# Optimization experiments

Measured on AMD Instinct MI355X. Metric: run time of the kernel, lower is better.

Reference implementation:

```python
import jax, jax.numpy as jnp
import numpy as np

OFFSETS = (1, 2, 4, 8, 16, 64, 96, 192, 384, 512, 768, 1024)
J = 12
J_LARGE = 8  # offsets with index >= 4 use phase rotation


def _shift(x, d):
    """Return x shifted so out[..., n, :] = x[..., n-d, :]; zeros where n < d.
    Shift is along axis 2 (the sequence axis of [B,H,N,...])."""
    pad = [(0, 0)] * x.ndim
    pad[2] = (d, 0)
    return jnp.pad(x, pad)[:, :, : x.shape[2]]


def setup_inputs() -> dict:
    key = jax.random.key(0)
    ks = jax.random.split(key, 9)
    B, H, N, HD = 2, 16, 4096, 64
    f = jnp.float32
    q = jax.random.normal(ks[0], (B, H, N, HD), f)
    k = jax.random.normal(ks[1], (B, H, N, HD), f)
    v = jax.random.normal(ks[2], (B, H, N, HD), f)
    pb = jax.random.normal(ks[3], (J, H), f) * 0.1          # per-offset per-head score bias
    se = jax.random.normal(ks[4], (J, HD), f) * 0.1         # per-offset score embedding
    phase_base = jax.random.normal(ks[5], (J_LARGE, H, 2), f) * 0.1
    phase_gain = jax.random.normal(ks[6], (J_LARGE, H, 2), f) * 0.1
    y_pre = jax.random.normal(ks[7], (B, H, N, 2), f)       # query-side phase features
    z_pre = jax.random.normal(ks[8], (B, H, N, 2), f)       # key-side phase features
    return dict(q=q, k=k, v=v, pb=pb, se=se, phase_base=phase_base,
                phase_gain=phase_gain, y_pre=y_pre, z_pre=z_pre)


def reference(q, k, v, pb, se, phase_base, phase_gain, y_pre, z_pre):
    B, H, N, HD = q.shape
    sc = 1.0 / float(np.sqrt(HD))
    n_idx = jnp.arange(N)

    # --- scores over the J fixed causal offsets: s_i[n] = (q_n . (k_{n-d} + se_i)) * sc + pb[i,h]
    scores = []
    for i, d in enumerate(OFFSETS):
        ks_ = _shift(k, d)  # key at n - d
        s = (jnp.einsum('bhnd,bhnd->bhn', q, ks_)
             + jnp.einsum('bhnd,d->bhn', q, se[i])) * sc
        s = s + pb[i][None, :, None]
        valid = (n_idx >= d)[None, None, :]
        scores.append(jnp.where(valid, s, -jnp.inf))
    scores = jnp.stack(scores, axis=-1)  # [B,H,N,J]

    lse = jax.nn.logsumexp(scores, axis=-1)            # [B,H,N]
    safe_lse = jnp.where(jnp.isfinite(lse), lse, 0.0)  # rows with no valid offset -> alpha = 0
    alpha = jnp.exp(scores - safe_lse[..., None])      # [B,H,N,J]; -inf scores give exactly 0

    # --- weighted sum of (phase-rotated) values
    out = jnp.zeros_like(q)
    for i, d in enumerate(OFFSETS):
        vs = _shift(v, d)  # value at n - d: [B,H,N,HD]
        if i >= 4:
            pi = i - 4
            zs = _shift(z_pre, d)  # key-side phase features at n - d: [B,H,N,2]
            # theta_p = base[pi,h,p] + gain[pi,h,p] * y_pre[n,p] * z_pre[n-d,p]
            theta = (phase_base[pi][None, :, None, :]
                     + phase_gain[pi][None, :, None, :] * y_pre * zs)  # [B,H,N,2]
            c, s_ = jnp.cos(theta), jnp.sin(theta)
            v0, v1, v2, v3 = vs[..., 0], vs[..., 1], vs[..., 2], vs[..., 3]
            rot = jnp.stack([c[..., 0] * v0 - s_[..., 0] * v1,
                             s_[..., 0] * v0 + c[..., 0] * v1,
                             c[..., 1] * v2 - s_[..., 1] * v3,
                             s_[..., 1] * v2 + c[..., 1] * v3], axis=-1)
            vs = jnp.concatenate([rot, vs[..., 4:]], axis=-1)
        out = out + alpha[..., i:i + 1] * vs
    return out
```

## Files before the change

### kernel.cpp

```cpp
#include <hip/hip_runtime.h>


namespace {

constexpr int J   = 12;
constexpr int B_  = 2;
constexpr int H_  = 16;
constexpr int N_  = 4096;
constexpr int HD_ = 64;
constexpr int OFFS[J] = {1, 2, 4, 8, 16, 64, 96, 192, 384, 512, 768, 1024};
constexpr int T_  = 64;
constexpr int W_  = 80;

using f32x4 = __attribute__((ext_vector_type(4))) float;
using f32x2 = __attribute__((ext_vector_type(2))) float;

#define GLOAD4(dst, off, base)                                              \
    asm volatile("global_load_dwordx4 %0, %1, %2"                           \
                 : "=v"(dst) : "v"(off), "s"(base) : "memory")
#define GLOAD2(dst, off, base)                                              \
    asm volatile("global_load_dwordx2 %0, %1, %2"                           \
                 : "=v"(dst) : "v"(off), "s"(base) : "memory")

#define VMWAIT(N)                                                           \
    asm volatile("s_waitcnt vmcnt(" #N ")" ::: "memory");                   \
    __builtin_amdgcn_sched_barrier(0)

template <int CTRL>
__device__ __forceinline__ float dpp_add(float x) {
    int s = __builtin_amdgcn_update_dpp(0, __builtin_bit_cast(int, x),
                                        CTRL, 0xF, 0xF, false);
    return x + __builtin_bit_cast(float, s);
}

#define ISSUEA(nn, QR, KR, YP, ZL) do {                                     \
    const int nA_ = (nn);                                                   \
    const uint32_t rbA_ = ((uint32_t)nA_ << 8) + gbl;                       \
    GLOAD4(QR, rbA_, qb);                                                   \
    _Pragma("unroll")                                                       \
    for (int i = 5; i < J; ++i) {                                           \
        const uint32_t oA_ = (nA_ >= OFFS[i])                               \
            ? (rbA_ - ((uint32_t)OFFS[i] << 8)) : gbl;                      \
        GLOAD4(KR[i - 5], oA_, kb);                                         \
    }                                                                       \
    const uint32_t nb8A_ = (uint32_t)nA_ << 3;                              \
    GLOAD2(YP, nb8A_, yb);                                                  \
    const uint32_t zoA_ = (nA_ >= dl) ? ((uint32_t)(nA_ - dl) << 3) : 0u;   \
    GLOAD2(ZL, zoA_, zb);                                                   \
} while (0)

#define ITERBODY(NVAL, TOPN, TAILN, PREF, QR, KR, YP, ZL, QRN, KRN, YPN, ZLN) \
do {                                                                        \
    const int n_ = (NVAL);                                                  \
    const uint32_t rowb_ = ((uint32_t)n_ << 8) + gbl;                       \
    VMWAIT(TOPN);                                   \
    const int rbase_ = n_ - P + 16;                        \
    float p_[J];                                                            \
    _Pragma("unroll")                                                       \
    for (int i = 0; i < 5; ++i) {                                           \
        const f32x4 kk  = kS[(rbase_ - OFFS[i]) * 16 + grp];                \
        const f32x4 seg = seS[i * 16 + grp];                                \
        float t = QR.x * (kk.x + seg.x);                                    \
        t = fmaf(QR.y, kk.y + seg.y, t);                                    \
        t = fmaf(QR.z, kk.z + seg.z, t);                                    \
        p_[i] = fmaf(QR.w, kk.w + seg.w, t);                                \
    }                                                                       \
    _Pragma("unroll")                                                       \
    for (int i = 5; i < J; ++i) {                                           \
        const f32x4 kk  = KR[i - 5];                                        \
        const f32x4 seg = seS[i * 16 + grp];                                \
        float t = QR.x * (kk.x + seg.x);                                    \
        t = fmaf(QR.y, kk.y + seg.y, t);                                    \
        t = fmaf(QR.z, kk.z + seg.z, t);                                    \
        p_[i] = fmaf(QR.w, kk.w + seg.w, t);                                \
    }                                                                       \
                  \
    f32x4 vr_[7];                                                           \
    _Pragma("unroll")                                                       \
    for (int i = 5; i < J; ++i) {                                           \
        const uint32_t oB_ = (n_ >= OFFS[i])                                \
            ? (rowb_ - ((uint32_t)OFFS[i] << 8)) : gbl;                     \
        GLOAD4(vr_[i - 5], oB_, vb);                                        \
    }                                                                       \
    f32x4 vx_;                                                              \
    const uint32_t vxo_ = (n_ >= dl) ? ((uint32_t)(n_ - dl) << 8) : 0u;     \
    GLOAD4(vx_, vxo_, vb);                                                  \
    if (PREF) { ISSUEA(n_ + 4, QRN, KRN, YPN, ZLN); }                       \
          \
    _Pragma("unroll")                                                       \
    for (int i = 0; i < J; ++i) {                                           \
        p_[i] = dpp_add<0xB1>(p_[i]);      \
        p_[i] = dpp_add<0x4E>(p_[i]);      \
        p_[i] = dpp_add<0x124>(p_[i]);                       \
        p_[i] = dpp_add<0x128>(p_[i]);                       \
    }                                                                       \
    float e_[J];                                                            \
    float sum_ = 0.f;                                                       \
    _Pragma("unroll")                                                       \
    for (int i = 0; i < J; ++i) {                                           \
        const float si = fmaf(p_[i], 0.125f, pbh[i]);                       \
        e_[i] = (n_ >= OFFS[i]) ? __expf(si) : 0.f;                         \
        sum_ += e_[i];                                                      \
    }                                                                       \
    VMWAIT(TAILN);                  \
                \
    const float s01_ = (t8 & 1) ? e_[5]  : e_[4];                           \
    const float s23_ = (t8 & 1) ? e_[7]  : e_[6];                           \
    const float s45_ = (t8 & 1) ? e_[9]  : e_[8];                           \
    const float s67_ = (t8 & 1) ? e_[11] : e_[10];                          \
    const float sA_  = (t8 & 2) ? s23_ : s01_;                              \
    const float sB_  = (t8 & 2) ? s67_ : s45_;                              \
    const float esel_ = (t8 & 4) ? sB_ : sA_;                               \
    const float th0_ = fmaf(pgn.x, YP.x * ZL.x, pbs.x);                     \
    const float th1_ = fmaf(pgn.y, YP.y * ZL.y, pbs.y);                     \
    const float c0_ = __cosf(th0_), s0_ = __sinf(th0_);                     \
    const float c1_ = __cosf(th1_), s1_ = __sinf(th1_);                     \
    f32x4 cx_;                                                              \
    cx_.x = esel_ * (c0_ * vx_.x - s0_ * vx_.y);                            \
    cx_.y = esel_ * (s0_ * vx_.x + c0_ * vx_.y);                            \
    cx_.z = esel_ * (c1_ * vx_.z - s1_ * vx_.w);                            \
    cx_.w = esel_ * (s1_ * vx_.z + c1_ * vx_.w);                            \
    cx_.x = dpp_add<0xB1>(cx_.x);  cx_.y = dpp_add<0xB1>(cx_.y);            \
    cx_.z = dpp_add<0xB1>(cx_.z);  cx_.w = dpp_add<0xB1>(cx_.w);            \
    cx_.x = dpp_add<0x4E>(cx_.x);  cx_.y = dpp_add<0x4E>(cx_.y);            \
    cx_.z = dpp_add<0x4E>(cx_.z);  cx_.w = dpp_add<0x4E>(cx_.w);            \
    cx_.x = dpp_add<0x124>(cx_.x); cx_.y = dpp_add<0x124>(cx_.y);           \
    cx_.z = dpp_add<0x124>(cx_.z); cx_.w = dpp_add<0x124>(cx_.w);           \
                     \
    float4 accl_ = make_float4(0.f, 0.f, 0.f, 0.f);                         \
    _Pragma("unroll")                                                       \
    for (int i = 0; i < 4; ++i) {                                           \
        const f32x4 vv = vS[(rbase_ - OFFS[i]) * 16 + grp];                 \
        accl_.x = fmaf(e_[i], vv.x, accl_.x);                               \
        accl_.y = fmaf(e_[i], vv.y, accl_.y);                               \
        accl_.z = fmaf(e_[i], vv.z, accl_.z);                               \
        accl_.w = fmaf(e_[i], vv.w, accl_.w);                               \
    }                                                                       \
    float4 acch_ = accl_;                                                   \
    {                                                                       \
        const f32x4 vv = vS[(rbase_ - 16) * 16 + grp];                      \
        acch_.x = fmaf(e_[4], vv.x, acch_.x);                               \
        acch_.y = fmaf(e_[4], vv.y, acch_.y);                               \
        acch_.z = fmaf(e_[4], vv.z, acch_.z);                               \
        acch_.w = fmaf(e_[4], vv.w, acch_.w);                               \
    }                                                                       \
    _Pragma("unroll")                                                       \
    for (int i = 5; i < J; ++i) {                                           \
        acch_.x = fmaf(e_[i], vr_[i - 5].x, acch_.x);                       \
        acch_.y = fmaf(e_[i], vr_[i - 5].y, acch_.y);                       \
        acch_.z = fmaf(e_[i], vr_[i - 5].z, acch_.z);                       \
        acch_.w = fmaf(e_[i], vr_[i - 5].w, acch_.w);                       \
    }                                                                       \
    const bool lo_ = (grp == 0);                                            \
    float4 acc_;                                                            \
    acc_.x = lo_ ? accl_.x + cx_.x : acch_.x;                               \
    acc_.y = lo_ ? accl_.y + cx_.y : acch_.y;                               \
    acc_.z = lo_ ? accl_.z + cx_.z : acch_.z;                               \
    acc_.w = lo_ ? accl_.w + cx_.w : acch_.w;                               \
    float4 res_;                                                            \
    if (n_ >= 1) {                                                          \
        const float inv_ = __builtin_amdgcn_rcpf(sum_);                     \
        res_ = make_float4(acc_.x * inv_, acc_.y * inv_,                    \
                           acc_.z * inv_, acc_.w * inv_);                   \
    } else {                                                                \
        res_ = make_float4(0.f, 0.f, 0.f, 0.f);                             \
    }                                                                       \
    *(float4*)(ob + rowb_) = res_;        \
} while (0)

__global__ __launch_bounds__(256, 3) void dsqg_kernel(
    const float* __restrict__ q, const float* __restrict__ k,
    const float* __restrict__ v, const float* __restrict__ pb,
    const float* __restrict__ se, const float* __restrict__ phase_base,
    const float* __restrict__ phase_gain, const float* __restrict__ y_pre,
    const float* __restrict__ z_pre, float* __restrict__ out)
{
    __shared__ f32x4 kS[W_ * 16];
    __shared__ f32x4 vS[W_ * 16];
    __shared__ f32x4 seS[J * 16];

    const int raw = blockIdx.x;
    const int per = gridDim.x >> 3;
    const int wid = (raw & 7) * per + (raw >> 3);

    const int bh  = wid >> 6;
    const int blk = wid & 63;
    const int h   = bh & (H_ - 1);
    const int P   = blk * T_;

    const int tid  = threadIdx.x;
    const int lane = tid & 63;
    const int wave = tid >> 6;
    const int grp  = lane & 15;
    const int sub  = lane >> 4;

    if (tid < J * 16) seS[tid] = ((const f32x4*)se)[tid];

    const size_t bhbytes = (size_t)bh * (N_ * HD_ * 4);
    const char* qb = (const char*)q + bhbytes;
    const char* kb = (const char*)k + bhbytes;
    const char* vb = (const char*)v + bhbytes;
    char*       ob = (char*)out + bhbytes;
    const char* yb = (const char*)y_pre + (size_t)bh * (N_ * 8);
    const char* zb = (const char*)z_pre + (size_t)bh * (N_ * 8);

    {
        const int r0 = P - 16;
#pragma unroll
        for (int t = 0; t < (W_ * 16) / 256; ++t) {
            const int idx = t * 256 + tid;
            const int row = idx >> 4;
            const int col = idx & 15;
            int gr = r0 + row;
            gr = gr < 0 ? 0 : gr;
            const uint32_t go = ((uint32_t)gr << 8) + ((uint32_t)col << 4);
            kS[idx] = *(const f32x4*)(kb + go);
            vS[idx] = *(const f32x4*)(vb + go);
        }
    }

    const int t8  = grp & 7;
    const int d01 = (t8 & 1) ? 64   : 16;
    const int d23 = (t8 & 1) ? 192  : 96;
    const int d45 = (t8 & 1) ? 512  : 384;
    const int d67 = (t8 & 1) ? 1024 : 768;
    const int dA  = (t8 & 2) ? d23 : d01;
    const int dB  = (t8 & 2) ? d67 : d45;
    const int dl  = (t8 & 4) ? dB : dA;

    const uint32_t pofs = (uint32_t)(t8 * H_ + h) << 3;
    const f32x2 pbs = *(const f32x2*)((const char*)phase_base + pofs);
    const f32x2 pgn = *(const f32x2*)((const char*)phase_gain + pofs);
    float pbh[J];
#pragma unroll
    for (int i = 0; i < J; ++i) pbh[i] = pb[i * H_ + h];

    asm volatile("" :: "v"(pbs.x), "v"(pbs.y), "v"(pgn.x), "v"(pgn.y));
    asm volatile("" :: "v"(pbh[0]), "v"(pbh[1]), "v"(pbh[2]), "v"(pbh[3]),
                       "v"(pbh[4]), "v"(pbh[5]), "v"(pbh[6]), "v"(pbh[7]),
                       "v"(pbh[8]), "v"(pbh[9]), "v"(pbh[10]), "v"(pbh[11]));

    __syncthreads();

    const uint32_t gbl = (uint32_t)grp << 4;
    const int n0 = P + wave * 16 + sub;

    f32x4 qrA, qrB;
    f32x4 krA[7], krB[7];
    f32x2 ypA, ypB, zlA, zlB;

    ISSUEA(n0, qrA, krA, ypA, zlA);

    ITERBODY(n0,      2, 10, 1, qrA, krA, ypA, zlA, qrB, krB, ypB, zlB);
    ITERBODY(n0 + 4,  3, 10, 1, qrB, krB, ypB, zlB, qrA, krA, ypA, zlA);
    ITERBODY(n0 + 8,  3, 10, 1, qrA, krA, ypA, zlA, qrB, krB, ypB, zlB);
    ITERBODY(n0 + 12, 3,  0, 0, qrB, krB, ypB, zlB, qrA, krA, ypA, zlA);
}

}

extern "C" void kernel_launch(void* const* d_in, const int* in_sizes, int n_in,
                              void* d_out, int out_size, void* d_ws, size_t ws_size,
                              hipStream_t stream) {
    const float* q          = (const float*)d_in[0];
    const float* k          = (const float*)d_in[1];
    const float* v          = (const float*)d_in[2];
    const float* pb         = (const float*)d_in[3];
    const float* se         = (const float*)d_in[4];
    const float* phase_base = (const float*)d_in[5];
    const float* phase_gain = (const float*)d_in[6];
    const float* y_pre      = (const float*)d_in[7];
    const float* z_pre      = (const float*)d_in[8];
    float* out              = (float*)d_out;

    const int positions = B_ * H_ * N_;
    const int blocks    = positions / T_;
    dsqg_kernel<<<blocks, 256, 0, stream>>>(q, k, v, pb, se, phase_base,
                                            phase_gain, y_pre, z_pre, out);
}
```

Measured before the change: 173.7 us.

## Enlarge tiles and LDS halo so offsets up to 96 read K/V from shared memory

Raises the per-block tile from 64 to 128 positions, runs 512 threads per block, and widens the staged K/V halo to 96 rows. Offsets 64 and 96 now read keys and values from LDS instead of global memory, and some lanes fetch the rotated value from LDS. The row interleaving across waves and the prefetch stride change to match. The aim is fewer global K/V loads per position and better reuse. The cost is a larger dynamic LDS footprint (about 114 KB per block), which lowers occupancy, plus a bigger halo load per block.

```diff
diff --git a/kernel.cpp b/kernel.cpp
--- a/kernel.cpp
+++ b/kernel.cpp
@@ -9,8 +9,11 @@
 constexpr int N_  = 4096;
 constexpr int HD_ = 64;
 constexpr int OFFS[J] = {1, 2, 4, 8, 16, 64, 96, 192, 384, 512, 768, 1024};
-constexpr int T_  = 64;
-constexpr int W_  = 80;
+constexpr int T_   = 128;
+constexpr int HALO = 96;
+constexpr int W_   = T_ + HALO;
+constexpr int LDS_KV = W_ * 16 * 16;
+constexpr int LDS_TOTAL = 2 * LDS_KV + J * 16 * 16;
 
 using f32x4 = __attribute__((ext_vector_type(4))) float;
 using f32x2 = __attribute__((ext_vector_type(2))) float;
@@ -38,10 +41,10 @@
     const uint32_t rbA_ = ((uint32_t)nA_ << 8) + gbl;                       \
     GLOAD4(QR, rbA_, qb);                                                   \
     _Pragma("unroll")                                                       \
-    for (int i = 5; i < J; ++i) {                                           \
+    for (int i = 7; i < J; ++i) {                                           \
         const uint32_t oA_ = (nA_ >= OFFS[i])                               \
             ? (rbA_ - ((uint32_t)OFFS[i] << 8)) : gbl;                      \
-        GLOAD4(KR[i - 5], oA_, kb);                                         \
+        GLOAD4(KR[i - 7], oA_, kb);                                         \
     }                                                                       \
     const uint32_t nb8A_ = (uint32_t)nA_ << 3;                              \
     GLOAD2(YP, nb8A_, yb);                                                  \
@@ -54,10 +57,10 @@
     const int n_ = (NVAL);                                                  \
     const uint32_t rowb_ = ((uint32_t)n_ << 8) + gbl;                       \
     VMWAIT(TOPN);                                   \
-    const int rbase_ = n_ - P + 16;                        \
+    const int rbase_ = n_ - P + HALO;                     \
     float p_[J];                                                            \
     _Pragma("unroll")                                                       \
-    for (int i = 0; i < 5; ++i) {                                           \
+    for (int i = 0; i < 7; ++i) {                \
         const f32x4 kk  = kS[(rbase_ - OFFS[i]) * 16 + grp];                \
         const f32x4 seg = seS[i * 16 + grp];                                \
         float t = QR.x * (kk.x + seg.x);                                    \
@@ -66,26 +69,27 @@
         p_[i] = fmaf(QR.w, kk.w + seg.w, t);                                \
     }                                                                       \
     _Pragma("unroll")                                                       \
-    for (int i = 5; i < J; ++i) {                                           \
-        const f32x4 kk  = KR[i - 5];                                        \
+    for (int i = 7; i < J; ++i) {                    \
+        const f32x4 kk  = KR[i - 7];                                        \
         const f32x4 seg = seS[i * 16 + grp];                                \
         float t = QR.x * (kk.x + seg.x);                                    \
         t = fmaf(QR.y, kk.y + seg.y, t);                                    \
         t = fmaf(QR.z, kk.z + seg.z, t);                                    \
         p_[i] = fmaf(QR.w, kk.w + seg.w, t);                                \
     }                                                                       \
-                  \
-    f32x4 vr_[7];                                                           \
-    _Pragma("unroll")                                                       \
-    for (int i = 5; i < J; ++i) {                                           \
+                             \
+    f32x4 vr_[5];                                                           \
+    _Pragma("unroll")                                                       \
+    for (int i = 7; i < J; ++i) {                                           \
         const uint32_t oB_ = (n_ >= OFFS[i])                                \
             ? (rowb_ - ((uint32_t)OFFS[i] << 8)) : gbl;                     \
-        GLOAD4(vr_[i - 5], oB_, vb);                                        \
-    }                                                                       \
-    f32x4 vx_;                                                              \
-    const uint32_t vxo_ = (n_ >= dl) ? ((uint32_t)(n_ - dl) << 8) : 0u;     \
-    GLOAD4(vx_, vxo_, vb);                                                  \
-    if (PREF) { ISSUEA(n_ + 4, QRN, KRN, YPN, ZLN); }                       \
+        GLOAD4(vr_[i - 7], oB_, vb);                                        \
+    }                                                                       \
+    f32x4 vxg_;                                                             \
+    const uint32_t vxo_ = ((t8 >= 3) && (n_ >= dl))                         \
+        ? ((uint32_t)(n_ - dl) << 8) : 0u;                                  \
+    GLOAD4(vxg_, vxo_, vb);                                                 \
+    if (PREF) { ISSUEA(n_ + 32, QRN, KRN, YPN, ZLN); }                      \
           \
     _Pragma("unroll")                                                       \
     for (int i = 0; i < J; ++i) {                                           \
@@ -102,7 +106,11 @@
         e_[i] = (n_ >= OFFS[i]) ? __expf(si) : 0.f;                         \
         sum_ += e_[i];                                                      \
     }                                                                       \
+              \
+    const int relv_ = (t8 <= 2) ? (rbase_ - dl) : 0;                        \
+    const f32x4 vxl_ = vS[relv_ * 16];                                      \
     VMWAIT(TAILN);                  \
+    const f32x4 vx_ = (t8 <= 2) ? vxl_ : vxg_;                              \
                 \
     const float s01_ = (t8 & 1) ? e_[5]  : e_[4];                           \
     const float s23_ = (t8 & 1) ? e_[7]  : e_[6];                           \
@@ -137,19 +145,20 @@
         accl_.w = fmaf(e_[i], vv.w, accl_.w);                               \
     }                                                                       \
     float4 acch_ = accl_;                                                   \
-    {                                                                       \
-        const f32x4 vv = vS[(rbase_ - 16) * 16 + grp];                      \
-        acch_.x = fmaf(e_[4], vv.x, acch_.x);                               \
-        acch_.y = fmaf(e_[4], vv.y, acch_.y);                               \
-        acch_.z = fmaf(e_[4], vv.z, acch_.z);                               \
-        acch_.w = fmaf(e_[4], vv.w, acch_.w);                               \
-    }                                                                       \
-    _Pragma("unroll")                                                       \
-    for (int i = 5; i < J; ++i) {                                           \
-        acch_.x = fmaf(e_[i], vr_[i - 5].x, acch_.x);                       \
-        acch_.y = fmaf(e_[i], vr_[i - 5].y, acch_.y);                       \
-        acch_.z = fmaf(e_[i], vr_[i - 5].z, acch_.z);                       \
-        acch_.w = fmaf(e_[i], vr_[i - 5].w, acch_.w);                       \
+    _Pragma("unroll")                                                       \
+    for (int i = 4; i < 7; ++i) {                 \
+        const f32x4 vv = vS[(rbase_ - OFFS[i]) * 16 + grp];                 \
+        acch_.x = fmaf(e_[i], vv.x, acch_.x);                               \
+        acch_.y = fmaf(e_[i], vv.y, acch_.y);                               \
+        acch_.z = fmaf(e_[i], vv.z, acch_.z);                               \
+        acch_.w = fmaf(e_[i], vv.w, acch_.w);                               \
+    }                                                                       \
+    _Pragma("unroll")                                                       \
+    for (int i = 7; i < J; ++i) {                                           \
+        acch_.x = fmaf(e_[i], vr_[i - 7].x, acch_.x);                       \
+        acch_.y = fmaf(e_[i], vr_[i - 7].y, acch_.y);                       \
+        acch_.z = fmaf(e_[i], vr_[i - 7].z, acch_.z);                       \
+        acch_.w = fmaf(e_[i], vr_[i - 7].w, acch_.w);                       \
     }                                                                       \
     const bool lo_ = (grp == 0);                                            \
     float4 acc_;                                                            \
@@ -168,23 +177,24 @@
     *(float4*)(ob + rowb_) = res_;        \
 } while (0)
 
-__global__ __launch_bounds__(256, 3) void dsqg_kernel(
+__global__ __launch_bounds__(512, 2) void dsqg_kernel(
     const float* __restrict__ q, const float* __restrict__ k,
     const float* __restrict__ v, const float* __restrict__ pb,
     const float* __restrict__ se, const float* __restrict__ phase_base,
     const float* __restrict__ phase_gain, const float* __restrict__ y_pre,
     const float* __restrict__ z_pre, float* __restrict__ out)
 {
-    __shared__ f32x4 kS[W_ * 16];
-    __shared__ f32x4 vS[W_ * 16];
-    __shared__ f32x4 seS[J * 16];
+    extern __shared__ char smem[];
+    f32x4* kS  = (f32x4*)smem;
+    f32x4* vS  = (f32x4*)(smem + LDS_KV);
+    f32x4* seS = (f32x4*)(smem + 2 * LDS_KV);
 
     const int raw = blockIdx.x;
     const int per = gridDim.x >> 3;
     const int wid = (raw & 7) * per + (raw >> 3);
 
-    const int bh  = wid >> 6;
-    const int blk = wid & 63;
+    const int bh  = wid >> 5;
+    const int blk = wid & 31;
     const int h   = bh & (H_ - 1);
     const int P   = blk * T_;
 
@@ -205,10 +215,10 @@
     const char* zb = (const char*)z_pre + (size_t)bh * (N_ * 8);
 
     {
-        const int r0 = P - 16;
+        const int r0 = P - HALO;
 #pragma unroll
-        for (int t = 0; t < (W_ * 16) / 256; ++t) {
-            const int idx = t * 256 + tid;
+        for (int t = 0; t < (W_ * 16) / 512; ++t) {
+            const int idx = t * 512 + tid;
             const int row = idx >> 4;
             const int col = idx & 15;
             int gr = r0 + row;
@@ -243,18 +253,18 @@
     __syncthreads();
 
     const uint32_t gbl = (uint32_t)grp << 4;
-    const int n0 = P + wave * 16 + sub;
+    const int n0 = P + wave * 4 + sub;
 
     f32x4 qrA, qrB;
-    f32x4 krA[7], krB[7];
+    f32x4 krA[5], krB[5];
     f32x2 ypA, ypB, zlA, zlB;
 
     ISSUEA(n0, qrA, krA, ypA, zlA);
 
-    ITERBODY(n0,      2, 10, 1, qrA, krA, ypA, zlA, qrB, krB, ypB, zlB);
-    ITERBODY(n0 + 4,  3, 10, 1, qrB, krB, ypB, zlB, qrA, krA, ypA, zlA);
-    ITERBODY(n0 + 8,  3, 10, 1, qrA, krA, ypA, zlA, qrB, krB, ypB, zlB);
-    ITERBODY(n0 + 12, 3,  0, 0, qrB, krB, ypB, zlB, qrA, krA, ypA, zlA);
+    ITERBODY(n0,      2, 8, 1, qrA, krA, ypA, zlA, qrB, krB, ypB, zlB);
+    ITERBODY(n0 + 32, 3, 8, 1, qrB, krB, ypB, zlB, qrA, krA, ypA, zlA);
+    ITERBODY(n0 + 64, 3, 8, 1, qrA, krA, ypA, zlA, qrB, krB, ypB, zlB);
+    ITERBODY(n0 + 96, 3, 0, 0, qrB, krB, ypB, zlB, qrA, krA, ypA, zlA);
 }
 
 }
@@ -273,8 +283,17 @@
     const float* z_pre      = (const float*)d_in[8];
     float* out              = (float*)d_out;
 
+    static bool attr_set = false;
+    if (!attr_set) {
+        (void)hipFuncSetAttribute((const void*)dsqg_kernel,
+                                  hipFuncAttributeMaxDynamicSharedMemorySize,
+                                  LDS_TOTAL);
+        attr_set = true;
+    }
+
     const int positions = B_ * H_ * N_;
     const int blocks    = positions / T_;
-    dsqg_kernel<<<blocks, 256, 0, stream>>>(q, k, v, pb, se, phase_base,
-                                            phase_gain, y_pre, z_pre, out);
-}
+    dsqg_kernel<<<blocks, 512, LDS_TOTAL, stream>>>(q, k, v, pb, se,
+                                                    phase_base, phase_gain,
+                                                    y_pre, z_pre, out);
+}
```

Result: no change. 173.0 us (-0.4%).

## Software-pipeline V loads and epilogue one row behind score computation

Applied to the files above, without the earlier changes.

Splits the per-row body into separate stages: K load, dot product, V/phase load, softmax and epilogue. The epilogue for row n now runs after the scores for row n+4 are computed, so V loads have a full iteration to land instead of being waited on right after issue. Q/K registers are single-buffered while V, phase and exp buffers are double-buffered. Launch bounds drop from 3 to 2 blocks per SIMD to make room for the extra live registers, which lowers occupancy in exchange for more in-flight loads per wave.

```diff
diff --git a/kernel.cpp b/kernel.cpp
--- a/kernel.cpp
+++ b/kernel.cpp
@@ -33,60 +33,59 @@
     return x + __builtin_bit_cast(float, s);
 }
 
-#define ISSUEA(nn, QR, KR, YP, ZL) do {                                     \
+#define ISSUEA(nn) do {                                                     \
     const int nA_ = (nn);                                                   \
     const uint32_t rbA_ = ((uint32_t)nA_ << 8) + gbl;                       \
-    GLOAD4(QR, rbA_, qb);                                                   \
+    GLOAD4(qr, rbA_, qb);                                                   \
     _Pragma("unroll")                                                       \
     for (int i = 5; i < J; ++i) {                                           \
         const uint32_t oA_ = (nA_ >= OFFS[i])                               \
             ? (rbA_ - ((uint32_t)OFFS[i] << 8)) : gbl;                      \
-        GLOAD4(KR[i - 5], oA_, kb);                                         \
-    }                                                                       \
-    const uint32_t nb8A_ = (uint32_t)nA_ << 3;                              \
-    GLOAD2(YP, nb8A_, yb);                                                  \
-    const uint32_t zoA_ = (nA_ >= dl) ? ((uint32_t)(nA_ - dl) << 3) : 0u;   \
-    GLOAD2(ZL, zoA_, zb);                                                   \
-} while (0)
-
-#define ITERBODY(NVAL, TOPN, TAILN, PREF, QR, KR, YP, ZL, QRN, KRN, YPN, ZLN) \
-do {                                                                        \
-    const int n_ = (NVAL);                                                  \
-    const uint32_t rowb_ = ((uint32_t)n_ << 8) + gbl;                       \
-    VMWAIT(TOPN);                                   \
-    const int rbase_ = n_ - P + 16;                        \
-    float p_[J];                                                            \
+        GLOAD4(kr[i - 5], oA_, kb);                                         \
+    }                                                                       \
+} while (0)
+
+#define ISSUEB(nn, VR, VX, YP, ZL) do {                                     \
+    const int nB_ = (nn);                                                   \
+    const uint32_t rbB_ = ((uint32_t)nB_ << 8) + gbl;                       \
+    _Pragma("unroll")                                                       \
+    for (int i = 5; i < J; ++i) {                                           \
+        const uint32_t oB_ = (nB_ >= OFFS[i])                               \
+            ? (rbB_ - ((uint32_t)OFFS[i] << 8)) : gbl;                      \
+        GLOAD4(VR[i - 5], oB_, vb);                                         \
+    }                                                                       \
+    const uint32_t vxo_ = (nB_ >= dl) ? ((uint32_t)(nB_ - dl) << 8) : 0u;   \
+    GLOAD4(VX, vxo_, vb);                                                   \
+    const uint32_t nb8_ = (uint32_t)nB_ << 3;                               \
+    GLOAD2(YP, nb8_, yb);                                                   \
+    const uint32_t zo_ = (nB_ >= dl) ? ((uint32_t)(nB_ - dl) << 3) : 0u;    \
+    GLOAD2(ZL, zo_, zb);                                                    \
+} while (0)
+
+#define DOTP(nn) do {                                                       \
+    const int nD_ = (nn);                                                   \
+    const int rbD_ = nD_ - P + 16;                         \
     _Pragma("unroll")                                                       \
     for (int i = 0; i < 5; ++i) {                                           \
-        const f32x4 kk  = kS[(rbase_ - OFFS[i]) * 16 + grp];                \
-        const f32x4 seg = seS[i * 16 + grp];                                \
-        float t = QR.x * (kk.x + seg.x);                                    \
-        t = fmaf(QR.y, kk.y + seg.y, t);                                    \
-        t = fmaf(QR.z, kk.z + seg.z, t);                                    \
-        p_[i] = fmaf(QR.w, kk.w + seg.w, t);                                \
+        const f32x4 kk = kS[(rbD_ - OFFS[i]) * 16 + grp];                   \
+        const f32x4 sg = seS[i * 16 + grp];                                 \
+        float t = qr.x * (kk.x + sg.x);                                     \
+        t = fmaf(qr.y, kk.y + sg.y, t);                                     \
+        t = fmaf(qr.z, kk.z + sg.z, t);                                     \
+        p_[i] = fmaf(qr.w, kk.w + sg.w, t);                                 \
     }                                                                       \
     _Pragma("unroll")                                                       \
     for (int i = 5; i < J; ++i) {                                           \
-        const f32x4 kk  = KR[i - 5];                                        \
-        const f32x4 seg = seS[i * 16 + grp];                                \
-        float t = QR.x * (kk.x + seg.x);                                    \
-        t = fmaf(QR.y, kk.y + seg.y, t);                                    \
-        t = fmaf(QR.z, kk.z + seg.z, t);                                    \
-        p_[i] = fmaf(QR.w, kk.w + seg.w, t);                                \
-    }                                                                       \
-                  \
-    f32x4 vr_[7];                                                           \
-    _Pragma("unroll")                                                       \
-    for (int i = 5; i < J; ++i) {                                           \
-        const uint32_t oB_ = (n_ >= OFFS[i])                                \
-            ? (rowb_ - ((uint32_t)OFFS[i] << 8)) : gbl;                     \
-        GLOAD4(vr_[i - 5], oB_, vb);                                        \
-    }                                                                       \
-    f32x4 vx_;                                                              \
-    const uint32_t vxo_ = (n_ >= dl) ? ((uint32_t)(n_ - dl) << 8) : 0u;     \
-    GLOAD4(vx_, vxo_, vb);                                                  \
-    if (PREF) { ISSUEA(n_ + 4, QRN, KRN, YPN, ZLN); }                       \
-          \
+        const f32x4 kk = kr[i - 5];                                         \
+        const f32x4 sg = seS[i * 16 + grp];                                 \
+        float t = qr.x * (kk.x + sg.x);                                     \
+        t = fmaf(qr.y, kk.y + sg.y, t);                                     \
+        t = fmaf(qr.z, kk.z + sg.z, t);                                     \
+        p_[i] = fmaf(qr.w, kk.w + sg.w, t);                                 \
+    }                                                                       \
+} while (0)
+
+#define SOFTMAXE(nn, E, SUM) do {                                           \
     _Pragma("unroll")                                                       \
     for (int i = 0; i < J; ++i) {                                           \
         p_[i] = dpp_add<0xB1>(p_[i]);      \
@@ -94,20 +93,23 @@
         p_[i] = dpp_add<0x124>(p_[i]);                       \
         p_[i] = dpp_add<0x128>(p_[i]);                       \
     }                                                                       \
-    float e_[J];                                                            \
-    float sum_ = 0.f;                                                       \
+    SUM = 0.f;                                                              \
     _Pragma("unroll")                                                       \
     for (int i = 0; i < J; ++i) {                                           \
         const float si = fmaf(p_[i], 0.125f, pbh[i]);                       \
-        e_[i] = (n_ >= OFFS[i]) ? __expf(si) : 0.f;                         \
-        sum_ += e_[i];                                                      \
-    }                                                                       \
-    VMWAIT(TAILN);                  \
-                \
-    const float s01_ = (t8 & 1) ? e_[5]  : e_[4];                           \
-    const float s23_ = (t8 & 1) ? e_[7]  : e_[6];                           \
-    const float s45_ = (t8 & 1) ? e_[9]  : e_[8];                           \
-    const float s67_ = (t8 & 1) ? e_[11] : e_[10];                          \
+        E[i] = ((nn) >= OFFS[i]) ? __expf(si) : 0.f;                        \
+        SUM += E[i];                                                        \
+    }                                                                       \
+} while (0)
+
+#define EPILOGUE(nn, VR, VX, YP, ZL, E, SUM) do {                           \
+    const int nE_ = (nn);                                                   \
+    const int rbE_ = nE_ - P + 16;                                          \
+    const uint32_t rowbE_ = ((uint32_t)nE_ << 8) + gbl;                     \
+    const float s01_ = (t8 & 1) ? E[5]  : E[4];                             \
+    const float s23_ = (t8 & 1) ? E[7]  : E[6];                             \
+    const float s45_ = (t8 & 1) ? E[9]  : E[8];                             \
+    const float s67_ = (t8 & 1) ? E[11] : E[10];                            \
     const float sA_  = (t8 & 2) ? s23_ : s01_;                              \
     const float sB_  = (t8 & 2) ? s67_ : s45_;                              \
     const float esel_ = (t8 & 4) ? sB_ : sA_;                               \
@@ -116,40 +118,39 @@
     const float c0_ = __cosf(th0_), s0_ = __sinf(th0_);                     \
     const float c1_ = __cosf(th1_), s1_ = __sinf(th1_);                     \
     f32x4 cx_;                                                              \
-    cx_.x = esel_ * (c0_ * vx_.x - s0_ * vx_.y);                            \
-    cx_.y = esel_ * (s0_ * vx_.x + c0_ * vx_.y);                            \
-    cx_.z = esel_ * (c1_ * vx_.z - s1_ * vx_.w);                            \
-    cx_.w = esel_ * (s1_ * vx_.z + c1_ * vx_.w);                            \
+    cx_.x = esel_ * (c0_ * VX.x - s0_ * VX.y);                              \
+    cx_.y = esel_ * (s0_ * VX.x + c0_ * VX.y);                              \
+    cx_.z = esel_ * (c1_ * VX.z - s1_ * VX.w);                              \
+    cx_.w = esel_ * (s1_ * VX.z + c1_ * VX.w);                              \
     cx_.x = dpp_add<0xB1>(cx_.x);  cx_.y = dpp_add<0xB1>(cx_.y);            \
     cx_.z = dpp_add<0xB1>(cx_.z);  cx_.w = dpp_add<0xB1>(cx_.w);            \
     cx_.x = dpp_add<0x4E>(cx_.x);  cx_.y = dpp_add<0x4E>(cx_.y);            \
     cx_.z = dpp_add<0x4E>(cx_.z);  cx_.w = dpp_add<0x4E>(cx_.w);            \
     cx_.x = dpp_add<0x124>(cx_.x); cx_.y = dpp_add<0x124>(cx_.y);           \
     cx_.z = dpp_add<0x124>(cx_.z); cx_.w = dpp_add<0x124>(cx_.w);           \
-                     \
     float4 accl_ = make_float4(0.f, 0.f, 0.f, 0.f);                         \
     _Pragma("unroll")                                                       \
     for (int i = 0; i < 4; ++i) {                                           \
-        const f32x4 vv = vS[(rbase_ - OFFS[i]) * 16 + grp];                 \
-        accl_.x = fmaf(e_[i], vv.x, accl_.x);                               \
-        accl_.y = fmaf(e_[i], vv.y, accl_.y);                               \
-        accl_.z = fmaf(e_[i], vv.z, accl_.z);                               \
-        accl_.w = fmaf(e_[i], vv.w, accl_.w);                               \
+        const f32x4 vv = vS[(rbE_ - OFFS[i]) * 16 + grp];                   \
+        accl_.x = fmaf(E[i], vv.x, accl_.x);                                \
+        accl_.y = fmaf(E[i], vv.y, accl_.y);                                \
+        accl_.z = fmaf(E[i], vv.z, accl_.z);                                \
+        accl_.w = fmaf(E[i], vv.w, accl_.w);                                \
     }                                                                       \
     float4 acch_ = accl_;                                                   \
-    {                                                                       \
-        const f32x4 vv = vS[(rbase_ - 16) * 16 + grp];                      \
-        acch_.x = fmaf(e_[4], vv.x, acch_.x);                               \
-        acch_.y = fmaf(e_[4], vv.y, acch_.y);                               \
-        acch_.z = fmaf(e_[4], vv.z, acch_.z);                               \
-        acch_.w = fmaf(e_[4], vv.w, acch_.w);                               \
+    {                                          \
+        const f32x4 vv = vS[(rbE_ - 16) * 16 + grp];                        \
+        acch_.x = fmaf(E[4], vv.x, acch_.x);                                \
+        acch_.y = fmaf(E[4], vv.y, acch_.y);                                \
+        acch_.z = fmaf(E[4], vv.z, acch_.z);                                \
+        acch_.w = fmaf(E[4], vv.w, acch_.w);                                \
     }                                                                       \
     _Pragma("unroll")                                                       \
     for (int i = 5; i < J; ++i) {                                           \
-        acch_.x = fmaf(e_[i], vr_[i - 5].x, acch_.x);                       \
-        acch_.y = fmaf(e_[i], vr_[i - 5].y, acch_.y);                       \
-        acch_.z = fmaf(e_[i], vr_[i - 5].z, acch_.z);                       \
-        acch_.w = fmaf(e_[i], vr_[i - 5].w, acch_.w);                       \
+        acch_.x = fmaf(E[i], VR[i - 5].x, acch_.x);                         \
+        acch_.y = fmaf(E[i], VR[i - 5].y, acch_.y);                         \
+        acch_.z = fmaf(E[i], VR[i - 5].z, acch_.z);                         \
+        acch_.w = fmaf(E[i], VR[i - 5].w, acch_.w);                         \
     }                                                                       \
     const bool lo_ = (grp == 0);                                            \
     float4 acc_;                                                            \
@@ -158,17 +159,17 @@
     acc_.z = lo_ ? accl_.z + cx_.z : acch_.z;                               \
     acc_.w = lo_ ? accl_.w + cx_.w : acch_.w;                               \
     float4 res_;                                                            \
-    if (n_ >= 1) {                                                          \
-        const float inv_ = __builtin_amdgcn_rcpf(sum_);                     \
+    if (nE_ >= 1) {                                                         \
+        const float inv_ = __builtin_amdgcn_rcpf(SUM);                      \
         res_ = make_float4(acc_.x * inv_, acc_.y * inv_,                    \
                            acc_.z * inv_, acc_.w * inv_);                   \
     } else {                                                                \
         res_ = make_float4(0.f, 0.f, 0.f, 0.f);                             \
     }                                                                       \
-    *(float4*)(ob + rowb_) = res_;        \
-} while (0)
-
-__global__ __launch_bounds__(256, 3) void dsqg_kernel(
+    *(float4*)(ob + rowbE_) = res_;                                         \
+} while (0)
+
+__global__ __launch_bounds__(256, 2) void dsqg_kernel(
     const float* __restrict__ q, const float* __restrict__ k,
     const float* __restrict__ v, const float* __restrict__ pb,
     const float* __restrict__ se, const float* __restrict__ phase_base,
@@ -235,26 +236,47 @@
 #pragma unroll
     for (int i = 0; i < J; ++i) pbh[i] = pb[i * H_ + h];
 
-    asm volatile("" :: "v"(pbs.x), "v"(pbs.y), "v"(pgn.x), "v"(pgn.y));
-    asm volatile("" :: "v"(pbh[0]), "v"(pbh[1]), "v"(pbh[2]), "v"(pbh[3]),
-                       "v"(pbh[4]), "v"(pbh[5]), "v"(pbh[6]), "v"(pbh[7]),
-                       "v"(pbh[8]), "v"(pbh[9]), "v"(pbh[10]), "v"(pbh[11]));
-
     __syncthreads();
 
     const uint32_t gbl = (uint32_t)grp << 4;
     const int n0 = P + wave * 16 + sub;
 
-    f32x4 qrA, qrB;
-    f32x4 krA[7], krB[7];
+    f32x4 qr;
+    f32x4 kr[7];
+    f32x4 vrA[7], vrB[7], vxA, vxB;
     f32x2 ypA, ypB, zlA, zlB;
-
-    ISSUEA(n0, qrA, krA, ypA, zlA);
-
-    ITERBODY(n0,      2, 10, 1, qrA, krA, ypA, zlA, qrB, krB, ypB, zlB);
-    ITERBODY(n0 + 4,  3, 10, 1, qrB, krB, ypB, zlB, qrA, krA, ypA, zlA);
-    ITERBODY(n0 + 8,  3, 10, 1, qrA, krA, ypA, zlA, qrB, krB, ypB, zlB);
-    ITERBODY(n0 + 12, 3,  0, 0, qrB, krB, ypB, zlB, qrA, krA, ypA, zlA);
+    float eA[J], eB[J], sumA, sumB;
+    float p_[J];
+
+    ISSUEA(n0);
+    VMWAIT(0);
+    DOTP(n0);
+    ISSUEB(n0, vrA, vxA, ypA, zlA);
+    ISSUEA(n0 + 4);
+    SOFTMAXE(n0, eA, sumA);
+
+    VMWAIT(0);
+    DOTP(n0 + 4);
+    ISSUEB(n0 + 4, vrB, vxB, ypB, zlB);
+    ISSUEA(n0 + 8);
+    SOFTMAXE(n0 + 4, eB, sumB);
+    EPILOGUE(n0, vrA, vxA, ypA, zlA, eA, sumA);
+
+    VMWAIT(1);
+    DOTP(n0 + 8);
+    ISSUEB(n0 + 8, vrA, vxA, ypA, zlA);
+    ISSUEA(n0 + 12);
+    SOFTMAXE(n0 + 8, eA, sumA);
+    EPILOGUE(n0 + 4, vrB, vxB, ypB, zlB, eB, sumB);
+
+    VMWAIT(1);
+    DOTP(n0 + 12);
+    ISSUEB(n0 + 12, vrB, vxB, ypB, zlB);
+    SOFTMAXE(n0 + 12, eB, sumB);
+    EPILOGUE(n0 + 8, vrA, vxA, ypA, zlA, eA, sumA);
+
+    VMWAIT(1);
+    EPILOGUE(n0 + 12, vrB, vxB, ypB, zlB, eB, sumB);
 }
 
 }
```

New measurement: 173.6 us. About the same (-0.1%).
